# Kernel tuning notes

Hardware: AMD Instinct MI355X
Metric: run time of the kernel (lower is better)

The kernel has to match this reference:

```python
import jax, jax.numpy as jnp
import numpy as np

B, S, T = 32, 128, 128
V, E, H = 32000, 256, 256
PAD_IDX = 0


def setup_inputs() -> dict:
    key = jax.random.key(0)
    ks = jax.random.split(key, 12)
    p = lambda k, shape: jax.random.normal(k, shape, dtype=jnp.float32) * 0.05
    src = jax.random.randint(ks[0], (B, S), 0, V)
    tgt = jax.random.randint(ks[1], (B, T), 0, V)
    enc_emb = p(ks[2], (V, E)).at[PAD_IDX].set(0.0)
    dec_emb = p(ks[3], (V, E)).at[PAD_IDX].set(0.0)
    return {
        'src': src,
        'tgt': tgt,
        'enc_emb': enc_emb,
        'enc_Wih': p(ks[4], (4 * H, E)),
        'enc_Whh': p(ks[5], (4 * H, H)),
        'enc_b': p(ks[6], (4 * H,)),
        'dec_emb': dec_emb,
        'dec_Wih': p(ks[7], (4 * H, E)),
        'dec_Whh': p(ks[8], (4 * H, H)),
        'dec_b': p(ks[9], (4 * H,)),
        'fc_W': p(ks[10], (V, H)),
        'fc_b': p(ks[11], (V,)),
    }


def lstm_scan(x_seq, h0, c0, Wih, Whh, b):
    # x_seq: [L, B, E] -> hs: [L, B, H]; PyTorch gate order i, f, g, o
    def step(carry, x):
        h, c = carry
        gates = x @ Wih.T + h @ Whh.T + b  # [B, 4H]
        i, f, g, o = jnp.split(gates, 4, axis=-1)
        c = jax.nn.sigmoid(f) * c + jax.nn.sigmoid(i) * jnp.tanh(g)
        h = jax.nn.sigmoid(o) * jnp.tanh(c)
        return (h, c), h
    (h, c), hs = jax.lax.scan(step, (h0, c0), x_seq)
    return hs, (h, c)


def reference(src, tgt, enc_emb, enc_Wih, enc_Whh, enc_b,
              dec_emb, dec_Wih, dec_Whh, dec_b, fc_W, fc_b):
    bs, tgt_len = tgt.shape
    # Encoder: embed + single-layer LSTM, keep final (h, c)
    x = jnp.swapaxes(enc_emb[src], 0, 1)            # [S, B, E]
    h0 = jnp.zeros((bs, enc_Whh.shape[1]), x.dtype)
    _, (h, c) = lstm_scan(x, h0, h0, enc_Wih, enc_Whh, enc_b)
    # Decoder with full teacher forcing (tf_ratio=1.0):
    # input at step t is tgt[:, t-1]; outputs[:, 0] stays zero.
    dec_in = jnp.swapaxes(dec_emb[tgt[:, :-1]], 0, 1)  # [T-1, B, E]
    hs, _ = lstm_scan(dec_in, h, c, dec_Wih, dec_Whh, dec_b)  # [T-1, B, H]
    logits = jnp.einsum('tbh,vh->btv', hs, fc_W) + fc_b        # [B, T-1, V]
    outputs = jnp.zeros((bs, tgt_len, fc_W.shape[0]), logits.dtype)
    return outputs.at[:, 1:].set(logits)
```

## Files before the change

### kernel.cpp

```cpp
#include <hip/hip_runtime.h>


typedef __attribute__((ext_vector_type(8))) short bf16x8;
typedef __attribute__((ext_vector_type(4))) float f32x4;
typedef __attribute__((ext_vector_type(8))) unsigned short u16x8;
typedef __attribute__((ext_vector_type(4))) unsigned int u32x4;
typedef __attribute__((ext_vector_type(8))) _Float16 f16x8;
typedef __attribute__((ext_vector_type(2))) _Float16 h2;

#define WS_XG_E   0u
#define WS_XG_D   16777216u
#define WS_FCW    33423360u
#define WS_HS     49807360u
#define WS_WTE    51904512u
#define WS_WTD    52428800u

#define KC_REG 48
#define KC_LDS 16

__device__ __forceinline__ unsigned short f2bf(float f) {
  unsigned u = __float_as_uint(f);
  u += 0x7FFFu + ((u >> 16) & 1u);
  return (unsigned short)(u >> 16);
}

__device__ __forceinline__ float sigf(float x) {
  float e = __expf(-x);
  return __builtin_amdgcn_rcpf(1.f + e);
}
__device__ __forceinline__ float tanh_fast(float x) {
  float e = __expf(-2.f * x);
  return fmaf(2.f, __builtin_amdgcn_rcpf(1.f + e), -1.f);
}

#if __has_builtin(__builtin_amdgcn_fdot2)
#define FDOT2(a, w, h) a = __builtin_amdgcn_fdot2(w, h, a, false)
#else
#define FDOT2(a, w, h) a = fmaf((float)w[0], (float)h[0], fmaf((float)w[1], (float)h[1], a))
#endif

__device__ __forceinline__ void dot8(const u16x8 w, const u32x4 hbits,
                                     float& a0, float& a1) {
  f16x8 wv = __builtin_bit_cast(f16x8, w);
  f16x8 hv = __builtin_bit_cast(f16x8, hbits);
  h2 w0 = {wv[0], wv[1]}, w1 = {wv[2], wv[3]};
  h2 w2 = {wv[4], wv[5]}, w3 = {wv[6], wv[7]};
  h2 h0 = {hv[0], hv[1]}, h1 = {hv[2], hv[3]};
  h2 hc = {hv[4], hv[5]}, h3 = {hv[6], hv[7]};
  FDOT2(a0, w0, h0);
  FDOT2(a1, w1, h1);
  FDOT2(a0, w2, hc);
  FDOT2(a1, w3, h3);
}

__global__ __launch_bounds__(256) void zero_col0(float* __restrict__ out) {
  int i = blockIdx.x * 256 + threadIdx.x;
  int b = i / 8000;
  int r = i - b * 8000;
  f32x4 z = {0.f, 0.f, 0.f, 0.f};
  __builtin_nontemporal_store(z, (f32x4*)out + b * 1024000 + r);
}

__global__ __launch_bounds__(256) void cvt_bf16(const float* __restrict__ in,
                                                unsigned short* __restrict__ o,
                                                int n4) {
  int i = blockIdx.x * 256 + threadIdx.x;
  if (i < n4) {
    float4 v = ((const float4*)in)[i];
    ushort4 u;
    u.x = f2bf(v.x); u.y = f2bf(v.y); u.z = f2bf(v.z); u.w = f2bf(v.w);
    *(ushort4*)(o + i * 4) = u;
  }
}

__global__ __launch_bounds__(256) void prep_whalf(const float* __restrict__ We,
                                                  const float* __restrict__ Wd,
                                                  unsigned short* __restrict__ Te,
                                                  unsigned short* __restrict__ Td) {
  int d = blockIdx.x * 256 + threadIdx.x;
  const float* W = blockIdx.y ? Wd : We;
  unsigned short* T = blockIdx.y ? Td : Te;
  int e = d & 7;
  int tmp = d >> 3;
  int tidb = tmp & 511;
  int j = tmp >> 9;
  int gg = j >> 4, kk = j & 15;
  int wv = tidb >> 6, ln = tidb & 63;
  int qq = ln >> 5, dm = wv * 32 + (ln & 31);
  _Float16 v = (_Float16)W[(gg * 256 + dm) * 256 + qq * 128 + kk * 8 + e];
  T[d] = __builtin_bit_cast(unsigned short, v);
}

__global__ __launch_bounds__(256) void xg_gemm(
    const int* __restrict__ tok, const float* __restrict__ emb,
    const float* __restrict__ Wih, const float* __restrict__ bias,
    float* __restrict__ xg, const int Mrows) {
  __shared__ unsigned short As[128][264];
  __shared__ unsigned short Bs[128][264];
  const int tid = threadIdx.x;
  const int nb = blockIdx.x, rb = blockIdx.y;
  {
    int lr = tid >> 1, half = tid & 1;
    int cb = half * 128;
    int row = rb * 128 + lr;
    int rowc = row < Mrows ? row : (Mrows - 1);
    int tt = rowc >> 5, bb = rowc & 31;
    int tk = tok[bb * 128 + tt];
    const float4* sa = (const float4*)(emb + tk * 256 + cb);
    const float4* sb = (const float4*)(Wih + (nb * 128 + lr) * 256 + cb);
#pragma unroll
    for (int i = 0; i < 32; ++i) {
      float4 v = sa[i];
      ushort4 u;
      u.x = f2bf(v.x); u.y = f2bf(v.y); u.z = f2bf(v.z); u.w = f2bf(v.w);
      *(ushort4*)&As[lr][cb + i * 4] = u;
      float4 v2 = sb[i];
      ushort4 u2;
      u2.x = f2bf(v2.x); u2.y = f2bf(v2.y); u2.z = f2bf(v2.z); u2.w = f2bf(v2.w);
      *(ushort4*)&Bs[lr][cb + i * 4] = u2;
    }
  }
  __syncthreads();
  const int lane = tid & 63, w = tid >> 6;
  const int wr = w >> 1, wc = w & 1;
  const int fr = lane & 15, kg = lane >> 4;
  f32x4 acc[4][4];
  const f32x4 zero = {0.f, 0.f, 0.f, 0.f};
#pragma unroll
  for (int mi = 0; mi < 4; ++mi)
#pragma unroll
    for (int ni = 0; ni < 4; ++ni) acc[mi][ni] = zero;
#pragma unroll
  for (int ks = 0; ks < 8; ++ks) {
    const int kb = ks * 32 + kg * 8;
    bf16x8 a[4], b[4];
#pragma unroll
    for (int mi = 0; mi < 4; ++mi)
      a[mi] = *(const bf16x8*)&As[wr * 64 + mi * 16 + fr][kb];
#pragma unroll
    for (int ni = 0; ni < 4; ++ni)
      b[ni] = *(const bf16x8*)&Bs[wc * 64 + ni * 16 + fr][kb];
#pragma unroll
    for (int mi = 0; mi < 4; ++mi)
#pragma unroll
      for (int ni = 0; ni < 4; ++ni)
        acc[mi][ni] = __builtin_amdgcn_mfma_f32_16x16x32_bf16(a[mi], b[ni], acc[mi][ni], 0, 0, 0);
  }
#pragma unroll
  for (int ni = 0; ni < 4; ++ni) {
    const int colg = nb * 128 + wc * 64 + ni * 16 + fr;
    const float bv = bias[colg];
#pragma unroll
    for (int mi = 0; mi < 4; ++mi) {
#pragma unroll
      for (int r = 0; r < 4; ++r) {
        int rowg = rb * 128 + wr * 64 + mi * 16 + kg * 4 + r;
        if (rowg < Mrows) xg[rowg * 1024 + colg] = acc[mi][ni][r] + bv;
      }
    }
  }
}

__global__ __launch_bounds__(512, 2) void lstm_batch(
    const unsigned short* __restrict__ WTe, const unsigned short* __restrict__ WTd,
    const float* __restrict__ xgE, const float* __restrict__ xgD,
    unsigned short* __restrict__ hs) {
  __shared__ __align__(16) unsigned short hh[2][256];
  __shared__ __align__(16) unsigned short wl[KC_LDS * 4096];
  const int tid = threadIdx.x;
  const int b = blockIdx.x;
  const int l = tid & 63, w = tid >> 6;
  const int q = l >> 5;
  const int dim = w * 32 + (l & 31);
  float c = 0.f;
  int cur = 0;
  if (tid < 256) hh[0][tid] = 0;

  for (int phase = 0; phase < 2; ++phase) {
    const unsigned short* WT = phase ? WTd : WTe;
    const float* xg = phase ? xgD : xgE;
    const int steps = phase ? 127 : 128;
    const u16x8* wsrc = (const u16x8*)WT + tid;
    u16x8 wr[KC_REG];
#pragma unroll
    for (int j = 0; j < KC_REG; ++j) wr[j] = wsrc[j * 512];
    __syncthreads();
    {
      u16x8* ld = (u16x8*)wl + tid;
#pragma unroll
      for (int j = 0; j < KC_LDS; ++j) ld[j * 512] = wsrc[(KC_REG + j) * 512];
    }
    __syncthreads();

    for (int t = 0; t < steps; ++t) {
      const float* xr = xg + (t * 32 + b) * 1024 + dim;
      float x0 = xr[0], x1 = xr[256], x2 = xr[512], x3 = xr[768];
      const u32x4* hq = (const u32x4*)&hh[cur][q * 128];
      const u16x8* wlp = (const u16x8*)wl + tid;
      float ai0 = 0.f, ai1 = 0.f, af0 = 0.f, af1 = 0.f;
      float ag0 = 0.f, ag1 = 0.f, ao0 = 0.f, ao1 = 0.f;
#pragma unroll
      for (int kk = 0; kk < 16; ++kk) {
        u32x4 hv = hq[kk];
        dot8(wr[kk],        hv, ai0, ai1);
        dot8(wr[16 + kk],   hv, af0, af1);
        dot8(wr[32 + kk],   hv, ag0, ag1);
        dot8(wlp[kk * 512], hv, ao0, ao1);
      }
      float gi = ai0 + ai1, gf = af0 + af1;
      float gg = ag0 + ag1, go = ao0 + ao1;
      gi += __shfl_xor(gi, 32, 64);
      gf += __shfl_xor(gf, 32, 64);
      gg += __shfl_xor(gg, 32, 64);
      go += __shfl_xor(go, 32, 64);
      gi += x0; gf += x1; gg += x2; go += x3;
      c = sigf(gf) * c + sigf(gi) * tanh_fast(gg);
      float h = sigf(go) * tanh_fast(c);
      if (l < 32) {
        _Float16 hf = (_Float16)h;
        hh[cur ^ 1][dim] = __builtin_bit_cast(unsigned short, hf);
        if (phase) hs[(b * 128 + t) * 256 + dim] = f2bf(h);
      }
      __syncthreads();
      cur ^= 1;
    }
  }
}

__global__ __launch_bounds__(256) void fc_gemm(
    const unsigned short* __restrict__ hsb, const unsigned short* __restrict__ fwb,
    const float* __restrict__ fcb, float* __restrict__ out) {
  __shared__ __align__(16) char smem[135168];
  typedef unsigned short usrow[264];
  usrow* As = (usrow*)smem;
  usrow* Bs = (usrow*)(smem + 128 * 264 * 2);
  const int tid = threadIdx.x;
  const int rb = blockIdx.x, nb = blockIdx.y;
  {
    int lr = tid >> 1, half = tid & 1;
    int cb = half * 128;
    const u16x8* s = (const u16x8*)(hsb + (rb * 128 + lr) * 256 + cb);
    const u16x8* s2 = (const u16x8*)(fwb + (nb * 128 + lr) * 256 + cb);
#pragma unroll
    for (int i = 0; i < 16; ++i) {
      *(u16x8*)&As[lr][cb + i * 8] = s[i];
      *(u16x8*)&Bs[lr][cb + i * 8] = s2[i];
    }
  }
  __syncthreads();
  const int lane = tid & 63, w = tid >> 6;
  const int wr = w >> 1, wc = w & 1;
  const int fr = lane & 15, kg = lane >> 4;
  f32x4 acc[4][4];
  const f32x4 zero = {0.f, 0.f, 0.f, 0.f};
#pragma unroll
  for (int mi = 0; mi < 4; ++mi)
#pragma unroll
    for (int ni = 0; ni < 4; ++ni) acc[mi][ni] = zero;
#pragma unroll
  for (int ks = 0; ks < 8; ++ks) {
    const int kb = ks * 32 + kg * 8;
    bf16x8 a[4], b[4];
#pragma unroll
    for (int mi = 0; mi < 4; ++mi)
      a[mi] = *(const bf16x8*)&As[wr * 64 + mi * 16 + fr][kb];
#pragma unroll
    for (int ni = 0; ni < 4; ++ni)
      b[ni] = *(const bf16x8*)&Bs[wc * 64 + ni * 16 + fr][kb];
#pragma unroll
    for (int mi = 0; mi < 4; ++mi)
#pragma unroll
      for (int ni = 0; ni < 4; ++ni)
        acc[mi][ni] = __builtin_amdgcn_mfma_f32_16x16x32_bf16(a[mi], b[ni], acc[mi][ni], 0, 0, 0);
  }
  __syncthreads();
  typedef float frow[132];
  frow* Ct = (frow*)smem;
#pragma unroll
  for (int ni = 0; ni < 4; ++ni) {
    const int cl = wc * 64 + ni * 16 + fr;
    const float bv = fcb[nb * 128 + cl];
#pragma unroll
    for (int mi = 0; mi < 4; ++mi) {
#pragma unroll
      for (int r = 0; r < 4; ++r)
        Ct[wr * 64 + mi * 16 + kg * 4 + r][cl] = acc[mi][ni][r] + bv;
    }
  }
  __syncthreads();
  const int rr = tid >> 5, cc = (tid & 31) * 4;
#pragma unroll
  for (int p = 0; p < 16; ++p) {
    int r = p * 8 + rr;
    if (r != 127) {
      float* dst = out + (size_t)(rb * 128 + r + 1) * 32000 + nb * 128 + cc;
      f32x4 v = *(const f32x4*)&Ct[r][cc];
      __builtin_nontemporal_store(v, (f32x4*)dst);
    }
  }
}

extern "C" void kernel_launch(void* const* d_in, const int* in_sizes, int n_in,
                              void* d_out, int out_size, void* d_ws, size_t ws_size,
                              hipStream_t stream) {
  const int* src = (const int*)d_in[0];
  const int* tgt = (const int*)d_in[1];
  const float* enc_emb = (const float*)d_in[2];
  const float* enc_Wih = (const float*)d_in[3];
  const float* enc_Whh = (const float*)d_in[4];
  const float* enc_b = (const float*)d_in[5];
  const float* dec_emb = (const float*)d_in[6];
  const float* dec_Wih = (const float*)d_in[7];
  const float* dec_Whh = (const float*)d_in[8];
  const float* dec_b = (const float*)d_in[9];
  const float* fc_W = (const float*)d_in[10];
  const float* fc_b = (const float*)d_in[11];
  float* out = (float*)d_out;
  char* ws = (char*)d_ws;

  float* xg_e = (float*)(ws + WS_XG_E);
  float* xg_d = (float*)(ws + WS_XG_D);
  unsigned short* fcw = (unsigned short*)(ws + WS_FCW);
  unsigned short* hs = (unsigned short*)(ws + WS_HS);
  unsigned short* wte = (unsigned short*)(ws + WS_WTE);
  unsigned short* wtd = (unsigned short*)(ws + WS_WTD);

  zero_col0<<<1000, 256, 0, stream>>>(out);
  cvt_bf16<<<8000, 256, 0, stream>>>(fc_W, fcw, 2048000);
  prep_whalf<<<dim3(1024, 2), 256, 0, stream>>>(enc_Whh, dec_Whh, wte, wtd);
  xg_gemm<<<dim3(8, 32), 256, 0, stream>>>(src, enc_emb, enc_Wih, enc_b, xg_e, 4096);
  xg_gemm<<<dim3(8, 32), 256, 0, stream>>>(tgt, dec_emb, dec_Wih, dec_b, xg_d, 4064);
  lstm_batch<<<32, 512, 0, stream>>>(wte, wtd, xg_e, xg_d, hs);
  fc_gemm<<<dim3(32, 250), 256, 0, stream>>>(hs, fcw, fc_b, out);
}
```

Measured before the change: 737.8 us.

## Fuse LSTM recurrence and FC projection into one persistent kernel with progress flags

Merges the LSTM recurrence and the output projection GEMM into a single persistent kernel of 256 blocks. The first 32 blocks run the recurrence and publish per-batch progress every 32 decoder steps. All blocks, including the LSTM blocks once they finish, pull 32x128 FC tiles from an atomic work counter and spin until the needed hidden states exist. The goal is to overlap the large logits write with the serial recurrence. In exchange it uses smaller tiles that reload the weight tiles more often, depends on all blocks being co-resident for the spin-waits, and adds atomic and spinning overhead.

```diff
diff --git a/kernel.cpp b/kernel.cpp
--- a/kernel.cpp
+++ b/kernel.cpp
@@ -14,9 +14,12 @@
 #define WS_HS     49807360u
 #define WS_WTE    51904512u
 #define WS_WTD    52428800u
+#define WS_FLAGS  52953088u
 
 #define KC_REG 48
 #define KC_LDS 16
+
+#define N_TILES 32000
 
 __device__ __forceinline__ unsigned short f2bf(float f) {
   unsigned u = __float_as_uint(f);
@@ -161,141 +164,162 @@
   }
 }
 
-__global__ __launch_bounds__(512, 2) void lstm_batch(
+__global__ __launch_bounds__(512, 2) void lstm_fc(
     const unsigned short* __restrict__ WTe, const unsigned short* __restrict__ WTd,
     const float* __restrict__ xgE, const float* __restrict__ xgD,
-    unsigned short* __restrict__ hs) {
-  __shared__ __align__(16) unsigned short hh[2][256];
-  __shared__ __align__(16) unsigned short wl[KC_LDS * 4096];
+    unsigned short* __restrict__ hs, const unsigned short* __restrict__ fwb,
+    const float* __restrict__ fcb, float* __restrict__ out,
+    unsigned* __restrict__ flags) {
+  __shared__ __align__(16) char smem[132096];
+  __shared__ int curid;
   const int tid = threadIdx.x;
-  const int b = blockIdx.x;
-  const int l = tid & 63, w = tid >> 6;
-  const int q = l >> 5;
-  const int dim = w * 32 + (l & 31);
-  float c = 0.f;
-  int cur = 0;
-  if (tid < 256) hh[0][tid] = 0;
-
-  for (int phase = 0; phase < 2; ++phase) {
-    const unsigned short* WT = phase ? WTd : WTe;
-    const float* xg = phase ? xgD : xgE;
-    const int steps = phase ? 127 : 128;
-    const u16x8* wsrc = (const u16x8*)WT + tid;
-    u16x8 wr[KC_REG];
-#pragma unroll
-    for (int j = 0; j < KC_REG; ++j) wr[j] = wsrc[j * 512];
-    __syncthreads();
-    {
-      u16x8* ld = (u16x8*)wl + tid;
-#pragma unroll
-      for (int j = 0; j < KC_LDS; ++j) ld[j * 512] = wsrc[(KC_REG + j) * 512];
-    }
-    __syncthreads();
-
-    for (int t = 0; t < steps; ++t) {
-      const float* xr = xg + (t * 32 + b) * 1024 + dim;
-      float x0 = xr[0], x1 = xr[256], x2 = xr[512], x3 = xr[768];
-      const u32x4* hq = (const u32x4*)&hh[cur][q * 128];
-      const u16x8* wlp = (const u16x8*)wl + tid;
-      float ai0 = 0.f, ai1 = 0.f, af0 = 0.f, af1 = 0.f;
-      float ag0 = 0.f, ag1 = 0.f, ao0 = 0.f, ao1 = 0.f;
-#pragma unroll
-      for (int kk = 0; kk < 16; ++kk) {
-        u32x4 hv = hq[kk];
-        dot8(wr[kk],        hv, ai0, ai1);
-        dot8(wr[16 + kk],   hv, af0, af1);
-        dot8(wr[32 + kk],   hv, ag0, ag1);
-        dot8(wlp[kk * 512], hv, ao0, ao1);
-      }
-      float gi = ai0 + ai1, gf = af0 + af1;
-      float gg = ag0 + ag1, go = ao0 + ao1;
-      gi += __shfl_xor(gi, 32, 64);
-      gf += __shfl_xor(gf, 32, 64);
-      gg += __shfl_xor(gg, 32, 64);
-      go += __shfl_xor(go, 32, 64);
-      gi += x0; gf += x1; gg += x2; go += x3;
-      c = sigf(gf) * c + sigf(gi) * tanh_fast(gg);
-      float h = sigf(go) * tanh_fast(c);
-      if (l < 32) {
-        _Float16 hf = (_Float16)h;
-        hh[cur ^ 1][dim] = __builtin_bit_cast(unsigned short, hf);
-        if (phase) hs[(b * 128 + t) * 256 + dim] = f2bf(h);
+  const int blk = blockIdx.x;
+  unsigned* prog = flags;
+  unsigned* ctr = flags + 32;
+
+  if (blk < 32) {
+    unsigned short (*hh)[256] = (unsigned short (*)[256])smem;
+    unsigned short* wl = (unsigned short*)(smem + 1024);
+    const int b = blk;
+    const int l = tid & 63, w = tid >> 6;
+    const int q = l >> 5;
+    const int dim = w * 32 + (l & 31);
+    float c = 0.f;
+    int cur = 0;
+    if (tid < 256) hh[0][tid] = 0;
+
+    for (int phase = 0; phase < 2; ++phase) {
+      const unsigned short* WT = phase ? WTd : WTe;
+      const float* xg = phase ? xgD : xgE;
+      const int steps = phase ? 127 : 128;
+      const u16x8* wsrc = (const u16x8*)WT + tid;
+      u16x8 wr[KC_REG];
+#pragma unroll
+      for (int j = 0; j < KC_REG; ++j) wr[j] = wsrc[j * 512];
+      __syncthreads();
+      {
+        u16x8* ld = (u16x8*)wl + tid;
+#pragma unroll
+        for (int j = 0; j < KC_LDS; ++j) ld[j * 512] = wsrc[(KC_REG + j) * 512];
       }
       __syncthreads();
-      cur ^= 1;
-    }
-  }
-}
-
-__global__ __launch_bounds__(256) void fc_gemm(
-    const unsigned short* __restrict__ hsb, const unsigned short* __restrict__ fwb,
-    const float* __restrict__ fcb, float* __restrict__ out) {
-  __shared__ __align__(16) char smem[135168];
+
+      for (int t = 0; t < steps; ++t) {
+        const float* xr = xg + (t * 32 + b) * 1024 + dim;
+        float x0 = xr[0], x1 = xr[256], x2 = xr[512], x3 = xr[768];
+        const u32x4* hq = (const u32x4*)&hh[cur][q * 128];
+        const u16x8* wlp = (const u16x8*)wl + tid;
+        float ai0 = 0.f, ai1 = 0.f, af0 = 0.f, af1 = 0.f;
+        float ag0 = 0.f, ag1 = 0.f, ao0 = 0.f, ao1 = 0.f;
+#pragma unroll
+        for (int kk = 0; kk < 16; ++kk) {
+          u32x4 hv = hq[kk];
+          dot8(wr[kk],        hv, ai0, ai1);
+          dot8(wr[16 + kk],   hv, af0, af1);
+          dot8(wr[32 + kk],   hv, ag0, ag1);
+          dot8(wlp[kk * 512], hv, ao0, ao1);
+        }
+        float gi = ai0 + ai1, gf = af0 + af1;
+        float gg = ag0 + ag1, go = ao0 + ao1;
+        gi += __shfl_xor(gi, 32, 64);
+        gf += __shfl_xor(gf, 32, 64);
+        gg += __shfl_xor(gg, 32, 64);
+        go += __shfl_xor(go, 32, 64);
+        gi += x0; gf += x1; gg += x2; go += x3;
+        c = sigf(gf) * c + sigf(gi) * tanh_fast(gg);
+        float h = sigf(go) * tanh_fast(c);
+        if (l < 32) {
+          _Float16 hf = (_Float16)h;
+          hh[cur ^ 1][dim] = __builtin_bit_cast(unsigned short, hf);
+          if (phase) hs[(b * 128 + t) * 256 + dim] = f2bf(h);
+        }
+        __syncthreads();
+        cur ^= 1;
+        if (phase && (((t & 31) == 31) || (t == 126))) {
+          if (tid == 0) {
+            __threadfence();
+            __hip_atomic_store(&prog[b], (unsigned)((t >> 5) + 1),
+                               __ATOMIC_RELEASE, __HIP_MEMORY_SCOPE_AGENT);
+          }
+        }
+      }
+    }
+  }
+
   typedef unsigned short usrow[264];
-  usrow* As = (usrow*)smem;
-  usrow* Bs = (usrow*)(smem + 128 * 264 * 2);
-  const int tid = threadIdx.x;
-  const int rb = blockIdx.x, nb = blockIdx.y;
-  {
-    int lr = tid >> 1, half = tid & 1;
-    int cb = half * 128;
-    const u16x8* s = (const u16x8*)(hsb + (rb * 128 + lr) * 256 + cb);
-    const u16x8* s2 = (const u16x8*)(fwb + (nb * 128 + lr) * 256 + cb);
-#pragma unroll
-    for (int i = 0; i < 16; ++i) {
-      *(u16x8*)&As[lr][cb + i * 8] = s[i];
-      *(u16x8*)&Bs[lr][cb + i * 8] = s2[i];
-    }
-  }
-  __syncthreads();
-  const int lane = tid & 63, w = tid >> 6;
-  const int wr = w >> 1, wc = w & 1;
+  usrow* Bs = (usrow*)smem;
+  usrow* As = (usrow*)(smem + 67584);
+  typedef float frow[132];
+  frow* Ct = (frow*)(smem + 67584);
+  const int lane = tid & 63, wv = tid >> 6;
+  const int wm = wv & 1, wn = wv >> 1;
   const int fr = lane & 15, kg = lane >> 4;
-  f32x4 acc[4][4];
-  const f32x4 zero = {0.f, 0.f, 0.f, 0.f};
-#pragma unroll
-  for (int mi = 0; mi < 4; ++mi)
-#pragma unroll
-    for (int ni = 0; ni < 4; ++ni) acc[mi][ni] = zero;
-#pragma unroll
-  for (int ks = 0; ks < 8; ++ks) {
-    const int kb = ks * 32 + kg * 8;
-    bf16x8 a[4], b[4];
-#pragma unroll
-    for (int mi = 0; mi < 4; ++mi)
-      a[mi] = *(const bf16x8*)&As[wr * 64 + mi * 16 + fr][kb];
-#pragma unroll
-    for (int ni = 0; ni < 4; ++ni)
-      b[ni] = *(const bf16x8*)&Bs[wc * 64 + ni * 16 + fr][kb];
-#pragma unroll
-    for (int mi = 0; mi < 4; ++mi)
-#pragma unroll
-      for (int ni = 0; ni < 4; ++ni)
-        acc[mi][ni] = __builtin_amdgcn_mfma_f32_16x16x32_bf16(a[mi], b[ni], acc[mi][ni], 0, 0, 0);
-  }
-  __syncthreads();
-  typedef float frow[132];
-  frow* Ct = (frow*)smem;
-#pragma unroll
-  for (int ni = 0; ni < 4; ++ni) {
-    const int cl = wc * 64 + ni * 16 + fr;
-    const float bv = fcb[nb * 128 + cl];
-#pragma unroll
-    for (int mi = 0; mi < 4; ++mi) {
+
+  while (true) {
+    __syncthreads();
+    if (tid == 0) {
+      curid = (int)__hip_atomic_fetch_add(ctr, 1u, __ATOMIC_RELAXED,
+                                          __HIP_MEMORY_SCOPE_AGENT);
+    }
+    __syncthreads();
+    const int id = curid;
+    if (id >= N_TILES) break;
+    const int tc = id / 8000;
+    const int rem = id - tc * 8000;
+    const int b = rem / 250, nb = rem - b * 250;
+    if (tid == 0) {
+      const unsigned need = (unsigned)(tc + 1);
+      while (__hip_atomic_load(&prog[b], __ATOMIC_RELAXED,
+                               __HIP_MEMORY_SCOPE_AGENT) < need)
+        __builtin_amdgcn_s_sleep(8);
+      (void)__hip_atomic_load(&prog[b], __ATOMIC_ACQUIRE,
+                              __HIP_MEMORY_SCOPE_AGENT);
+    }
+    __syncthreads();
+    {
+      int row = tid >> 2, sg = tid & 3;
+      const u16x8* s = (const u16x8*)(fwb + (nb * 128 + row) * 256 + sg * 64);
+      u16x8* d = (u16x8*)&Bs[row][sg * 64];
+#pragma unroll
+      for (int i = 0; i < 8; ++i) d[i] = s[i];
+      int ar = tid >> 4, ac = (tid & 15) * 16;
+      const u16x8* s2 = (const u16x8*)(hs + (b * 128 + tc * 32 + ar) * 256 + ac);
+      u16x8* d2 = (u16x8*)&As[ar][ac];
+      d2[0] = s2[0]; d2[1] = s2[1];
+    }
+    __syncthreads();
+    f32x4 acc[2];
+    const f32x4 zero = {0.f, 0.f, 0.f, 0.f};
+    acc[0] = zero; acc[1] = zero;
+#pragma unroll
+    for (int ks = 0; ks < 8; ++ks) {
+      const int kb = ks * 32 + kg * 8;
+      bf16x8 a = *(const bf16x8*)&As[wm * 16 + fr][kb];
+      bf16x8 b0 = *(const bf16x8*)&Bs[wn * 32 + fr][kb];
+      bf16x8 b1 = *(const bf16x8*)&Bs[wn * 32 + 16 + fr][kb];
+      acc[0] = __builtin_amdgcn_mfma_f32_16x16x32_bf16(a, b0, acc[0], 0, 0, 0);
+      acc[1] = __builtin_amdgcn_mfma_f32_16x16x32_bf16(a, b1, acc[1], 0, 0, 0);
+    }
+    __syncthreads();
+#pragma unroll
+    for (int ni = 0; ni < 2; ++ni) {
+      const int cl = wn * 32 + ni * 16 + fr;
+      const float bv = fcb[nb * 128 + cl];
 #pragma unroll
       for (int r = 0; r < 4; ++r)
-        Ct[wr * 64 + mi * 16 + kg * 4 + r][cl] = acc[mi][ni][r] + bv;
-    }
-  }
-  __syncthreads();
-  const int rr = tid >> 5, cc = (tid & 31) * 4;
-#pragma unroll
-  for (int p = 0; p < 16; ++p) {
-    int r = p * 8 + rr;
-    if (r != 127) {
-      float* dst = out + (size_t)(rb * 128 + r + 1) * 32000 + nb * 128 + cc;
-      f32x4 v = *(const f32x4*)&Ct[r][cc];
-      __builtin_nontemporal_store(v, (f32x4*)dst);
+        Ct[wm * 16 + kg * 4 + r][cl] = acc[ni][r] + bv;
+    }
+    __syncthreads();
+    {
+      int r = tid >> 4, cc = (tid & 15) * 8;
+      int tg = tc * 32 + r;
+      if (tg != 127) {
+        float* dst = out + (size_t)(b * 128 + tg + 1) * 32000 + nb * 128 + cc;
+        f32x4 v0 = *(const f32x4*)&Ct[r][cc];
+        f32x4 v1 = *(const f32x4*)&Ct[r][cc + 4];
+        __builtin_nontemporal_store(v0, (f32x4*)dst);
+        __builtin_nontemporal_store(v1, (f32x4*)(dst + 4));
+      }
     }
   }
 }
@@ -324,12 +348,13 @@
   unsigned short* hs = (unsigned short*)(ws + WS_HS);
   unsigned short* wte = (unsigned short*)(ws + WS_WTE);
   unsigned short* wtd = (unsigned short*)(ws + WS_WTD);
-
+  unsigned* flags = (unsigned*)(ws + WS_FLAGS);
+
+  hipMemsetAsync(ws + WS_FLAGS, 0, 256, stream);
   zero_col0<<<1000, 256, 0, stream>>>(out);
   cvt_bf16<<<8000, 256, 0, stream>>>(fc_W, fcw, 2048000);
   prep_whalf<<<dim3(1024, 2), 256, 0, stream>>>(enc_Whh, dec_Whh, wte, wtd);
   xg_gemm<<<dim3(8, 32), 256, 0, stream>>>(src, enc_emb, enc_Wih, enc_b, xg_e, 4096);
   xg_gemm<<<dim3(8, 32), 256, 0, stream>>>(tgt, dec_emb, dec_Wih, dec_b, xg_d, 4064);
-  lstm_batch<<<32, 512, 0, stream>>>(wte, wtd, xg_e, xg_d, hs);
-  fc_gemm<<<dim3(32, 250), 256, 0, stream>>>(hs, fcw, fc_b, out);
-}
+  lstm_fc<<<256, 512, 0, stream>>>(wte, wtd, xg_e, xg_d, hs, fcw, fc_b, out, flags);
+}
```

New measurement: 937.2 us. 27.0% more time.

## Process two batch rows per LSTM block and split FC GEMM K-loading into halves

Applied to the files above, without the earlier changes.

The LSTM recurrence kernel now handles two batch elements per workgroup, reusing each register/LDS-resident weight fragment for two hidden-state vectors. That halves the number of blocks (16 instead of 32) and gives each lane one batch's gate results after the cross-half shuffle. Separately, the FC GEMM stages K in two 128-wide chunks, halving its shared-memory footprint to allow more resident blocks, at the cost of an extra barrier pair. The LSTM change doubles the dot-product work per step per thread, which may lengthen the serial critical path.

```diff
diff --git a/kernel.cpp b/kernel.cpp
--- a/kernel.cpp
+++ b/kernel.cpp
@@ -39,18 +39,18 @@
 #define FDOT2(a, w, h) a = fmaf((float)w[0], (float)h[0], fmaf((float)w[1], (float)h[1], a))
 #endif
 
-__device__ __forceinline__ void dot8(const u16x8 w, const u32x4 hbits,
-                                     float& a0, float& a1) {
+__device__ __forceinline__ void dot8s(const u16x8 w, const u32x4 hbits,
+                                      float& a) {
   f16x8 wv = __builtin_bit_cast(f16x8, w);
   f16x8 hv = __builtin_bit_cast(f16x8, hbits);
   h2 w0 = {wv[0], wv[1]}, w1 = {wv[2], wv[3]};
   h2 w2 = {wv[4], wv[5]}, w3 = {wv[6], wv[7]};
   h2 h0 = {hv[0], hv[1]}, h1 = {hv[2], hv[3]};
   h2 hc = {hv[4], hv[5]}, h3 = {hv[6], hv[7]};
-  FDOT2(a0, w0, h0);
-  FDOT2(a1, w1, h1);
-  FDOT2(a0, w2, hc);
-  FDOT2(a1, w3, h3);
+  FDOT2(a, w0, h0);
+  FDOT2(a, w1, h1);
+  FDOT2(a, w2, hc);
+  FDOT2(a, w3, h3);
 }
 
 __global__ __launch_bounds__(256) void zero_col0(float* __restrict__ out) {
@@ -165,16 +165,16 @@
     const unsigned short* __restrict__ WTe, const unsigned short* __restrict__ WTd,
     const float* __restrict__ xgE, const float* __restrict__ xgD,
     unsigned short* __restrict__ hs) {
-  __shared__ __align__(16) unsigned short hh[2][256];
+  __shared__ __align__(16) unsigned short hh[2][2][256];
   __shared__ __align__(16) unsigned short wl[KC_LDS * 4096];
   const int tid = threadIdx.x;
-  const int b = blockIdx.x;
   const int l = tid & 63, w = tid >> 6;
   const int q = l >> 5;
   const int dim = w * 32 + (l & 31);
+  const int bq = blockIdx.x * 2 + q;
   float c = 0.f;
   int cur = 0;
-  if (tid < 256) hh[0][tid] = 0;
+  hh[0][tid >> 8][tid & 255] = 0;
 
   for (int phase = 0; phase < 2; ++phase) {
     const unsigned short* WT = phase ? WTd : WTe;
@@ -193,34 +193,37 @@
     __syncthreads();
 
     for (int t = 0; t < steps; ++t) {
-      const float* xr = xg + (t * 32 + b) * 1024 + dim;
+      const float* xr = xg + (t * 32 + bq) * 1024 + dim;
       float x0 = xr[0], x1 = xr[256], x2 = xr[512], x3 = xr[768];
-      const u32x4* hq = (const u32x4*)&hh[cur][q * 128];
+      const u32x4* hq0 = (const u32x4*)&hh[cur][0][q * 128];
+      const u32x4* hq1 = (const u32x4*)&hh[cur][1][q * 128];
       const u16x8* wlp = (const u16x8*)wl + tid;
-      float ai0 = 0.f, ai1 = 0.f, af0 = 0.f, af1 = 0.f;
-      float ag0 = 0.f, ag1 = 0.f, ao0 = 0.f, ao1 = 0.f;
+      float i0 = 0.f, f0 = 0.f, g0 = 0.f, o0 = 0.f;
+      float i1 = 0.f, f1 = 0.f, g1 = 0.f, o1 = 0.f;
 #pragma unroll
       for (int kk = 0; kk < 16; ++kk) {
-        u32x4 hv = hq[kk];
-        dot8(wr[kk],        hv, ai0, ai1);
-        dot8(wr[16 + kk],   hv, af0, af1);
-        dot8(wr[32 + kk],   hv, ag0, ag1);
-        dot8(wlp[kk * 512], hv, ao0, ao1);
+        u32x4 hv0 = hq0[kk];
+        u32x4 hv1 = hq1[kk];
+        u16x8 wi = wr[kk], wf = wr[16 + kk], wg = wr[32 + kk];
+        u16x8 wo = wlp[kk * 512];
+        dot8s(wi, hv0, i0); dot8s(wi, hv1, i1);
+        dot8s(wf, hv0, f0); dot8s(wf, hv1, f1);
+        dot8s(wg, hv0, g0); dot8s(wg, hv1, g1);
+        dot8s(wo, hv0, o0); dot8s(wo, hv1, o1);
       }
-      float gi = ai0 + ai1, gf = af0 + af1;
-      float gg = ag0 + ag1, go = ao0 + ao1;
-      gi += __shfl_xor(gi, 32, 64);
-      gf += __shfl_xor(gf, 32, 64);
-      gg += __shfl_xor(gg, 32, 64);
-      go += __shfl_xor(go, 32, 64);
-      gi += x0; gf += x1; gg += x2; go += x3;
+      i0 += __shfl_xor(i0, 32, 64); i1 += __shfl_xor(i1, 32, 64);
+      f0 += __shfl_xor(f0, 32, 64); f1 += __shfl_xor(f1, 32, 64);
+      g0 += __shfl_xor(g0, 32, 64); g1 += __shfl_xor(g1, 32, 64);
+      o0 += __shfl_xor(o0, 32, 64); o1 += __shfl_xor(o1, 32, 64);
+      float gi = (q ? i1 : i0) + x0;
+      float gf = (q ? f1 : f0) + x1;
+      float gg = (q ? g1 : g0) + x2;
+      float go = (q ? o1 : o0) + x3;
       c = sigf(gf) * c + sigf(gi) * tanh_fast(gg);
       float h = sigf(go) * tanh_fast(c);
-      if (l < 32) {
-        _Float16 hf = (_Float16)h;
-        hh[cur ^ 1][dim] = __builtin_bit_cast(unsigned short, hf);
-        if (phase) hs[(b * 128 + t) * 256 + dim] = f2bf(h);
-      }
+      _Float16 hf = (_Float16)h;
+      hh[cur ^ 1][q][dim] = __builtin_bit_cast(unsigned short, hf);
+      if (phase) hs[(bq * 128 + t) * 256 + dim] = f2bf(h);
       __syncthreads();
       cur ^= 1;
     }
@@ -230,24 +233,12 @@
 __global__ __launch_bounds__(256) void fc_gemm(
     const unsigned short* __restrict__ hsb, const unsigned short* __restrict__ fwb,
     const float* __restrict__ fcb, float* __restrict__ out) {
-  __shared__ __align__(16) char smem[135168];
-  typedef unsigned short usrow[264];
+  __shared__ __align__(16) char smem[69632];
+  typedef unsigned short usrow[136];
   usrow* As = (usrow*)smem;
-  usrow* Bs = (usrow*)(smem + 128 * 264 * 2);
+  usrow* Bs = (usrow*)(smem + 34816);
   const int tid = threadIdx.x;
   const int rb = blockIdx.x, nb = blockIdx.y;
-  {
-    int lr = tid >> 1, half = tid & 1;
-    int cb = half * 128;
-    const u16x8* s = (const u16x8*)(hsb + (rb * 128 + lr) * 256 + cb);
-    const u16x8* s2 = (const u16x8*)(fwb + (nb * 128 + lr) * 256 + cb);
-#pragma unroll
-    for (int i = 0; i < 16; ++i) {
-      *(u16x8*)&As[lr][cb + i * 8] = s[i];
-      *(u16x8*)&Bs[lr][cb + i * 8] = s2[i];
-    }
-  }
-  __syncthreads();
   const int lane = tid & 63, w = tid >> 6;
   const int wr = w >> 1, wc = w & 1;
   const int fr = lane & 15, kg = lane >> 4;
@@ -257,23 +248,37 @@
   for (int mi = 0; mi < 4; ++mi)
 #pragma unroll
     for (int ni = 0; ni < 4; ++ni) acc[mi][ni] = zero;
-#pragma unroll
-  for (int ks = 0; ks < 8; ++ks) {
-    const int kb = ks * 32 + kg * 8;
-    bf16x8 a[4], b[4];
-#pragma unroll
-    for (int mi = 0; mi < 4; ++mi)
-      a[mi] = *(const bf16x8*)&As[wr * 64 + mi * 16 + fr][kb];
-#pragma unroll
-    for (int ni = 0; ni < 4; ++ni)
-      b[ni] = *(const bf16x8*)&Bs[wc * 64 + ni * 16 + fr][kb];
-#pragma unroll
-    for (int mi = 0; mi < 4; ++mi)
+
+  const int lr = tid >> 1, half = tid & 1;
+#pragma unroll
+  for (int p = 0; p < 2; ++p) {
+    {
+      const u16x8* s = (const u16x8*)(hsb + (rb * 128 + lr) * 256 + p * 128 + half * 64);
+      const u16x8* s2 = (const u16x8*)(fwb + (nb * 128 + lr) * 256 + p * 128 + half * 64);
+      u16x8* d = (u16x8*)&As[lr][half * 64];
+      u16x8* d2 = (u16x8*)&Bs[lr][half * 64];
+#pragma unroll
+      for (int i = 0; i < 8; ++i) { d[i] = s[i]; d2[i] = s2[i]; }
+    }
+    __syncthreads();
+#pragma unroll
+    for (int ks = 0; ks < 4; ++ks) {
+      const int kb = ks * 32 + kg * 8;
+      bf16x8 a[4], b[4];
+#pragma unroll
+      for (int mi = 0; mi < 4; ++mi)
+        a[mi] = *(const bf16x8*)&As[wr * 64 + mi * 16 + fr][kb];
 #pragma unroll
       for (int ni = 0; ni < 4; ++ni)
-        acc[mi][ni] = __builtin_amdgcn_mfma_f32_16x16x32_bf16(a[mi], b[ni], acc[mi][ni], 0, 0, 0);
-  }
-  __syncthreads();
+        b[ni] = *(const bf16x8*)&Bs[wc * 64 + ni * 16 + fr][kb];
+#pragma unroll
+      for (int mi = 0; mi < 4; ++mi)
+#pragma unroll
+        for (int ni = 0; ni < 4; ++ni)
+          acc[mi][ni] = __builtin_amdgcn_mfma_f32_16x16x32_bf16(a[mi], b[ni], acc[mi][ni], 0, 0, 0);
+    }
+    __syncthreads();
+  }
   typedef float frow[132];
   frow* Ct = (frow*)smem;
 #pragma unroll
@@ -330,6 +335,6 @@
   prep_whalf<<<dim3(1024, 2), 256, 0, stream>>>(enc_Whh, dec_Whh, wte, wtd);
   xg_gemm<<<dim3(8, 32), 256, 0, stream>>>(src, enc_emb, enc_Wih, enc_b, xg_e, 4096);
   xg_gemm<<<dim3(8, 32), 256, 0, stream>>>(tgt, dec_emb, dec_Wih, dec_b, xg_d, 4064);
-  lstm_batch<<<32, 512, 0, stream>>>(wte, wtd, xg_e, xg_d, hs);
+  lstm_batch<<<16, 512, 0, stream>>>(wte, wtd, xg_e, xg_d, hs);
   fc_gemm<<<dim3(32, 250), 256, 0, stream>>>(hs, fcw, fc_b, out);
 }
```

Result: slower. 896.1 us (+21.5%).
